# Optimization experiments

Hardware: AMD Instinct MI355X
Metric: run time of the kernel (lower is better)

The kernel has to match this reference:

```python
import jax, jax.numpy as jnp
import numpy as np
from jax import lax

EMBED = 200
HID = 300
NCLASS = 2
B = 64
S = 255          # complete binary tree: 2**8 - 1 nodes
DEPTH = 8        # levels 0..7, root at node 0
VOCAB = 32000


def make_tree():
    parent = np.zeros(S, np.int32)
    parent[0] = S  # sentinel: root has no parent (dropped via dummy segment)
    for i in range(1, S):
        parent[i] = (i - 1) // 2
    depth = np.floor(np.log2(np.arange(S) + 1)).astype(np.int32)
    return jnp.asarray(parent), jnp.asarray(depth)


def setup_inputs() -> dict:
    key = jax.random.key(0)
    ks = jax.random.split(key, 8)
    parent, depth = make_tree()
    return {
        "x": jax.random.randint(ks[0], (S, B), 0, VOCAB, dtype=jnp.int32),
        "parent": parent,
        "depth": depth,
        "embed": jax.random.normal(ks[1], (VOCAB, EMBED), jnp.float32) * 0.1,
        "W_iou": jax.random.normal(ks[2], (EMBED, 3 * HID), jnp.float32) * 0.05,
        "U_iou": jax.random.normal(ks[3], (HID, 3 * HID), jnp.float32) * 0.05,
        "b_iou": jnp.zeros((3 * HID,), jnp.float32),
        "W_f": jax.random.normal(ks[4], (EMBED, HID), jnp.float32) * 0.05,
        "U_f": jax.random.normal(ks[5], (HID, HID), jnp.float32) * 0.05,
        "b_f": jnp.zeros((HID,), jnp.float32),
        "W_out": jax.random.normal(ks[6], (HID, NCLASS), jnp.float32) * 0.05,
        "b_out": jnp.zeros((NCLASS,), jnp.float32),
    }


def reference(x, parent, depth, embed, W_iou, U_iou, b_iou, W_f, U_f, b_f, W_out, b_out):
    # x: [S, B] token ids (seq-major, as in the torch model)
    emb = embed[x]                              # [S, B, E]
    wx_iou = emb @ W_iou + b_iou                # [S, B, 3H] input contributions
    wx_f = emb @ W_f + b_f                      # [S, B, H]
    seg = jnp.minimum(parent, S)                # root -> dummy segment S
    pidx = jnp.clip(parent, 0, S - 1)           # safe gather index for parent's x-part

    H0 = jnp.zeros((S, B, HID), emb.dtype)
    C0 = jnp.zeros((S, B, HID), emb.dtype)

    def level_step(carry, d):
        H, C = carry
        child = (depth == d + 1)[:, None, None].astype(H.dtype)   # nodes feeding level d
        # child-sum of hidden states into parents
        h_sum = jax.ops.segment_sum(H * child, seg, num_segments=S + 1)[:S]  # [S,B,H]
        # per-child forget gate: sigma(W_f x_parent + U_f h_child + b_f)
        f = jax.nn.sigmoid(wx_f[pidx] + H @ U_f)                  # [S,B,H]
        fc = jax.ops.segment_sum(f * C * child, seg, num_segments=S + 1)[:S]
        iou = wx_iou + h_sum @ U_iou                              # [S,B,3H]
        i_g, o_g, u_g = jnp.split(iou, 3, axis=-1)
        i_g = jax.nn.sigmoid(i_g)
        o_g = jax.nn.sigmoid(o_g)
        u_g = jnp.tanh(u_g)
        c_new = i_g * u_g + fc
        h_new = o_g * jnp.tanh(c_new)
        node = (depth == d)[:, None, None]
        H = jnp.where(node, h_new, H)
        C = jnp.where(node, c_new, C)
        return (H, C), None

    levels = jnp.arange(DEPTH - 1, -1, -1)      # process deepest level first
    (H, C), _ = lax.scan(level_step, (H0, C0), levels)

    tree_hidden = H[0]                          # [B, H] root hidden state
    logits = tree_hidden @ W_out + b_out        # Linear(hidden_dim, n_class)
    return jax.nn.log_softmax(logits, axis=-1)  # [B, 2]
```

## Files before the change

### kernel.cpp

```cpp
#include <hip/hip_runtime.h>
#include <hip/hip_bf16.h>
#include <math.h>

#define NS 255
#define NB 64
#define NE 200
#define NH 300
#define TS 2048


typedef __attribute__((ext_vector_type(8))) short short8;
typedef __attribute__((ext_vector_type(4))) float f32x4;

__device__ __forceinline__ float sigmoidf_(float x) { return 1.0f / (1.0f + __expf(-x)); }
__device__ __forceinline__ unsigned short f2bf(float v) {
    union { __hip_bfloat16 b; unsigned short u; } cv; cv.b = __float2bfloat16(v); return cv.u;
}
__device__ __forceinline__ float bf2f(unsigned short u) {
    union { unsigned short u; __hip_bfloat16 b; } cv; cv.u = u; return __bfloat162float(cv.b);
}
__device__ __forceinline__ int swz(int row, int kk) {
    int g = (kk >> 3) ^ ((row >> 1) & 3);
    return ((row << 2) + g) * 8 + (kk & 7);
}

__global__ __launch_bounds__(256) void prep_kernel(
    const float* __restrict__ U_iou, const float* __restrict__ U_f,
    const float* __restrict__ W_iou, const float* __restrict__ W_f,
    const float* __restrict__ embed, const int* __restrict__ x,
    unsigned short* __restrict__ BW, unsigned short* __restrict__ AembT)
{
    const int nBW = 4 * 5 * 17 * TS;
    const int nAe = NS * 7 * TS;
    int total = nBW + nAe;
    int stride = gridDim.x * blockDim.x;
    for (int i = blockIdx.x * blockDim.x + threadIdx.x; i < total; i += stride) {
        if (i < nBW) {
            int e = i & (TS - 1), tile = i >> 11;
            int c = tile % 17, t2 = tile / 17;
            int s = t2 % 5, g = t2 / 5;
            int row = e >> 5, pos = (e >> 3) & 3;
            int kk = ((pos ^ ((row >> 1) & 3)) << 3) + (e & 7);
            int j = s * 64 + row;
            float v = 0.f;
            if (c < 7) {
                int k = c * 32 + kk;
                if (j < NH && k < NE) v = (g < 3) ? W_iou[k * 900 + g * NH + j] : W_f[k * NH + j];
            } else {
                int k = (c - 7) * 32 + kk;
                if (j < NH && k < NH) v = (g < 3) ? U_iou[k * 900 + g * NH + j] : U_f[k * NH + j];
            }
            BW[i] = f2bf(v);
        } else {
            int i2 = i - nBW;
            int e = i2 & (TS - 1), tile = i2 >> 11;
            int c = tile % 7, node = tile / 7;
            int row = e >> 5, pos = (e >> 3) & 3;
            int kk = ((pos ^ ((row >> 1) & 3)) << 3) + (e & 7);
            int k = c * 32 + kk;
            float v = 0.f;
            if (k < NE) v = embed[(size_t)x[node * NB + row] * NE + k];
            AembT[i2] = f2bf(v);
        }
    }
}

template<int NCH>
__device__ __forceinline__ void gemm_h(f32x4 acc[4][2],
    const unsigned short* __restrict__ A, const unsigned short* __restrict__ B,
    int offA, int offB)
{
#pragma unroll
    for (int c = 0; c < NCH; ++c) {
        const unsigned short* At = A + c * TS + offA;
        const unsigned short* Bt = B + c * TS + offB;
        short8 a0 = *(const short8*)(At);
        short8 a1 = *(const short8*)(At + 512);
#pragma unroll
        for (int t = 0; t < 4; ++t) {
            short8 b = *(const short8*)(Bt + t * 512);
            acc[t][0] = __builtin_amdgcn_mfma_f32_16x16x32_bf16(a0, b, acc[t][0], 0, 0, 0);
            acc[t][1] = __builtin_amdgcn_mfma_f32_16x16x32_bf16(a1, b, acc[t][1], 0, 0, 0);
        }
    }
}

__global__ __launch_bounds__(320) void level_kernel(
    const unsigned short* __restrict__ AembT, const unsigned short* __restrict__ BW,
    const float* __restrict__ b_iou, const float* __restrict__ b_f,
    unsigned short* __restrict__ HbfT, float* __restrict__ C,
    int base, int m, int sh)
{
    int bid = blockIdx.x;
    int p, s, half;
    if (m > 0) {
        int xcd = bid & 7, idx = bid >> 3;
        int o = idx % m, rest = idx / m;
        p = base + xcd * m + o;
        s = rest % 5; half = rest / 5;
    } else {
        int xcd = bid & 7;
        if (xcd & ((1 << sh) - 1)) return;
        p = base + (xcd >> sh);
        int idx = bid >> 3;
        s = idx % 5; half = idx / 5;
    }
    int tid = threadIdx.x;
    int w = tid >> 6, lane = tid & 63, ln = lane & 15, quad = lane >> 4;
    int l = 2 * p + 1, r = 2 * p + 2;
    int bsel = (w < 4) ? w : 3;
    int g = (quad ^ ((ln >> 1) & 3)) * 8;
    int offA = (half * 32 + ln) * 32 + g;
    int offB = ln * 32 + g;

    const unsigned short* Bsrc = BW + (size_t)(bsel * 5 + s) * 17 * TS;
    const unsigned short* Ae = AembT + (size_t)p * 7 * TS;
    const unsigned short* Hl = HbfT + (size_t)l * 10 * TS;
    const unsigned short* Hr = HbfT + (size_t)r * 10 * TS;

    f32x4 acc[4][2];
#pragma unroll
    for (int t = 0; t < 4; ++t)
#pragma unroll
        for (int q = 0; q < 2; ++q) acc[t][q] = (f32x4){0.f, 0.f, 0.f, 0.f};

    if (w < 3) {
        gemm_h<7>(acc, Ae, Bsrc, offA, offB);
        gemm_h<10>(acc, Hl, Bsrc + 7 * TS, offA, offB);
        gemm_h<10>(acc, Hr, Bsrc + 7 * TS, offA, offB);
    } else {
        gemm_h<7>(acc, Ae, Bsrc, offA, offB);
        gemm_h<10>(acc, (w == 3) ? Hl : Hr, Bsrc + 7 * TS, offA, offB);
    }

    __shared__ float tile[5][32][17];
    for (int t = 0; t < 4; ++t) {
        __syncthreads();
#pragma unroll
        for (int ms = 0; ms < 2; ++ms)
#pragma unroll
            for (int rr = 0; rr < 4; ++rr)
                tile[w][ms * 16 + quad * 4 + rr][ln] = acc[t][ms][rr];
        __syncthreads();
        for (int idx = tid; idx < 512; idx += 320) {
            int mm = idx >> 4, n = idx & 15;
            int gm = half * 32 + mm;
            int jj = s * 64 + t * 16 + n;
            bool ok = jj < NH;
            float pi = tile[0][mm][n] + (ok ? b_iou[jj] : 0.f);
            float po = tile[1][mm][n] + (ok ? b_iou[NH + jj] : 0.f);
            float pu = tile[2][mm][n] + (ok ? b_iou[2 * NH + jj] : 0.f);
            float bj = ok ? b_f[jj] : 0.f;
            float fl = sigmoidf_(tile[3][mm][n] + bj);
            float fr = sigmoidf_(tile[4][mm][n] + bj);
            float cl = ok ? C[((size_t)l * NB + gm) * NH + jj] : 0.f;
            float cr = ok ? C[((size_t)r * NB + gm) * NH + jj] : 0.f;
            float cc = sigmoidf_(pi) * tanhf(pu) + fl * cl + fr * cr;
            float hh = sigmoidf_(po) * tanhf(cc);
            if (ok) C[((size_t)p * NB + gm) * NH + jj] = cc;
            HbfT[((size_t)p * 10 + (jj >> 5)) * TS + swz(gm, jj & 31)]
                = ok ? f2bf(hh) : (unsigned short)0;
        }
    }
}

__global__ __launch_bounds__(192) void leaf_kernel(
    const unsigned short* __restrict__ AembT, const unsigned short* __restrict__ BW,
    const float* __restrict__ b_iou,
    unsigned short* __restrict__ HbfT, float* __restrict__ C, int m)
{
    int bid = blockIdx.x;
    int xcd = bid & 7, idx = bid >> 3;
    int o = idx % m, rest = idx / m;
    int p = 127 + xcd * m + o;
    int s = rest % 5, half = rest / 5;
    int tid = threadIdx.x;
    int w = tid >> 6, lane = tid & 63, ln = lane & 15, quad = lane >> 4;
    int g = (quad ^ ((ln >> 1) & 3)) * 8;
    int offA = (half * 32 + ln) * 32 + g;
    int offB = ln * 32 + g;

    const unsigned short* Bsrc = BW + (size_t)(w * 5 + s) * 17 * TS;
    const unsigned short* Ae = AembT + (size_t)p * 7 * TS;

    f32x4 acc[4][2];
#pragma unroll
    for (int t = 0; t < 4; ++t)
#pragma unroll
        for (int q = 0; q < 2; ++q) acc[t][q] = (f32x4){0.f, 0.f, 0.f, 0.f};

    gemm_h<7>(acc, Ae, Bsrc, offA, offB);

    __shared__ float tile[3][32][17];
    for (int t = 0; t < 4; ++t) {
        __syncthreads();
#pragma unroll
        for (int ms = 0; ms < 2; ++ms)
#pragma unroll
            for (int rr = 0; rr < 4; ++rr)
                tile[w][ms * 16 + quad * 4 + rr][ln] = acc[t][ms][rr];
        __syncthreads();
        for (int idx2 = tid; idx2 < 512; idx2 += 192) {
            int mm = idx2 >> 4, n = idx2 & 15;
            int gm = half * 32 + mm;
            int jj = s * 64 + t * 16 + n;
            bool ok = jj < NH;
            float pi = tile[0][mm][n] + (ok ? b_iou[jj] : 0.f);
            float po = tile[1][mm][n] + (ok ? b_iou[NH + jj] : 0.f);
            float pu = tile[2][mm][n] + (ok ? b_iou[2 * NH + jj] : 0.f);
            float cc = sigmoidf_(pi) * tanhf(pu);
            float hh = sigmoidf_(po) * tanhf(cc);
            if (ok) C[((size_t)p * NB + gm) * NH + jj] = cc;
            HbfT[((size_t)p * 10 + (jj >> 5)) * TS + swz(gm, jj & 31)]
                = ok ? f2bf(hh) : (unsigned short)0;
        }
    }
}

__global__ __launch_bounds__(64) void out_kernel(
    const unsigned short* __restrict__ HbfT,
    const float* __restrict__ W_out, const float* __restrict__ b_out,
    float* __restrict__ out)
{
    int b = threadIdx.x;
    float l0 = 0.f, l1 = 0.f;
#pragma unroll 4
    for (int k = 0; k < NH; ++k) {
        float hk = bf2f(HbfT[(size_t)(k >> 5) * TS + swz(b, k & 31)]);
        l0 += hk * W_out[k * 2];
        l1 += hk * W_out[k * 2 + 1];
    }
    l0 += b_out[0];
    l1 += b_out[1];
    float m = fmaxf(l0, l1);
    float lse = m + logf(__expf(l0 - m) + __expf(l1 - m));
    out[b * 2 + 0] = l0 - lse;
    out[b * 2 + 1] = l1 - lse;
}

extern "C" void kernel_launch(void* const* d_in, const int* in_sizes, int n_in,
                              void* d_out, int out_size, void* d_ws, size_t ws_size,
                              hipStream_t stream)
{
    const int*   x     = (const int*)d_in[0];
    const float* embed = (const float*)d_in[3];
    const float* W_iou = (const float*)d_in[4];
    const float* U_iou = (const float*)d_in[5];
    const float* b_iou = (const float*)d_in[6];
    const float* W_f   = (const float*)d_in[7];
    const float* U_f   = (const float*)d_in[8];
    const float* b_f   = (const float*)d_in[9];
    const float* W_out = (const float*)d_in[10];
    const float* b_out = (const float*)d_in[11];

    char* ws = (char*)d_ws;
    unsigned short* HbfT  = (unsigned short*)(ws + 0);
    float*          C     = (float*)(ws + 10444800);
    unsigned short* AembT = (unsigned short*)(ws + 30028800);
    unsigned short* BW    = (unsigned short*)(ws + 37340160);

    prep_kernel<<<4096, 256, 0, stream>>>(U_iou, U_f, W_iou, W_f, embed, x, BW, AembT);

    leaf_kernel<<<1280, 192, 0, stream>>>(AembT, BW, b_iou, HbfT, C, 16);
    for (int d = 6; d >= 3; --d) {
        int base = (1 << d) - 1;
        int m = 1 << (d - 3);
        level_kernel<<<80 * m, 320, 0, stream>>>(AembT, BW, b_iou, b_f, HbfT, C,
                                                 base, m, 0);
    }
    for (int d = 2; d >= 0; --d) {
        level_kernel<<<80, 320, 0, stream>>>(AembT, BW, b_iou, b_f, HbfT, C,
                                             (1 << d) - 1, 0, 3 - d);
    }
    out_kernel<<<1, 64, 0, stream>>>(HbfT, W_out, b_out, (float*)d_out);
}
```

Before: 289.2 us.

## Store cell state in fp16 tiles, stage children via LDS, vectorize prep, widen leaf tiles

```diff
diff --git a/kernel.cpp b/kernel.cpp
--- a/kernel.cpp
+++ b/kernel.cpp
@@ -7,6 +7,7 @@
 #define NE 200
 #define NH 300
 #define TS 2048
+#define HTS 1024
 
 
 typedef __attribute__((ext_vector_type(8))) short short8;
@@ -18,6 +19,12 @@
 }
 __device__ __forceinline__ float bf2f(unsigned short u) {
     union { unsigned short u; __hip_bfloat16 b; } cv; cv.u = u; return __bfloat162float(cv.b);
+}
+__device__ __forceinline__ unsigned short f2h(float v) {
+    union { _Float16 h; unsigned short u; } cv; cv.h = (_Float16)v; return cv.u;
+}
+__device__ __forceinline__ float h2f(unsigned short u) {
+    union { unsigned short u; _Float16 h; } cv; cv.u = u; return (float)cv.h;
 }
 __device__ __forceinline__ int swz(int row, int kk) {
     int g = (kk >> 3) ^ ((row >> 1) & 3);
@@ -30,50 +37,58 @@
     const float* __restrict__ embed, const int* __restrict__ x,
     unsigned short* __restrict__ BW, unsigned short* __restrict__ AembT)
 {
-    const int nBW = 4 * 5 * 17 * TS;
-    const int nAe = NS * 7 * TS;
-    int total = nBW + nAe;
+    const int gBW = 4 * 5 * 17 * 256;
+    const int gAe = NS * 7 * 256;
+    int total = gBW + gAe;
     int stride = gridDim.x * blockDim.x;
-    for (int i = blockIdx.x * blockDim.x + threadIdx.x; i < total; i += stride) {
-        if (i < nBW) {
-            int e = i & (TS - 1), tile = i >> 11;
+    for (int gi = blockIdx.x * blockDim.x + threadIdx.x; gi < total; gi += stride) {
+        unsigned short st[8];
+        if (gi < gBW) {
+            int gg = gi & 255, tile = gi >> 8;
+            int row = gg >> 2, pos = gg & 3;
+            int kk0 = (pos ^ ((row >> 1) & 3)) << 3;
             int c = tile % 17, t2 = tile / 17;
-            int s = t2 % 5, g = t2 / 5;
-            int row = e >> 5, pos = (e >> 3) & 3;
-            int kk = ((pos ^ ((row >> 1) & 3)) << 3) + (e & 7);
+            int s = t2 % 5, g4 = t2 / 5;
             int j = s * 64 + row;
-            float v = 0.f;
-            if (c < 7) {
-                int k = c * 32 + kk;
-                if (j < NH && k < NE) v = (g < 3) ? W_iou[k * 900 + g * NH + j] : W_f[k * NH + j];
-            } else {
-                int k = (c - 7) * 32 + kk;
-                if (j < NH && k < NH) v = (g < 3) ? U_iou[k * 900 + g * NH + j] : U_f[k * NH + j];
+#pragma unroll
+            for (int u = 0; u < 8; ++u) {
+                int kk = kk0 + u; float v = 0.f;
+                if (c < 7) {
+                    int k = c * 32 + kk;
+                    if (j < NH && k < NE)
+                        v = (g4 < 3) ? W_iou[k * 900 + g4 * NH + j] : W_f[k * NH + j];
+                } else {
+                    int k = (c - 7) * 32 + kk;
+                    if (j < NH && k < NH)
+                        v = (g4 < 3) ? U_iou[k * 900 + g4 * NH + j] : U_f[k * NH + j];
+                }
+                st[u] = f2bf(v);
             }
-            BW[i] = f2bf(v);
+            *(short8*)(BW + (size_t)tile * TS + (row * 4 + pos) * 8) = *(short8*)st;
         } else {
-            int i2 = i - nBW;
-            int e = i2 & (TS - 1), tile = i2 >> 11;
+            int gi2 = gi - gBW;
+            int gg = gi2 & 255, tile = gi2 >> 8;
+            int row = gg >> 2, pos = gg & 3;
+            int kk0 = (pos ^ ((row >> 1) & 3)) << 3;
             int c = tile % 7, node = tile / 7;
-            int row = e >> 5, pos = (e >> 3) & 3;
-            int kk = ((pos ^ ((row >> 1) & 3)) << 3) + (e & 7);
-            int k = c * 32 + kk;
-            float v = 0.f;
-            if (k < NE) v = embed[(size_t)x[node * NB + row] * NE + k];
-            AembT[i2] = f2bf(v);
-        }
-    }
-}
-
-template<int NCH>
-__device__ __forceinline__ void gemm_h(f32x4 acc[4][2],
-    const unsigned short* __restrict__ A, const unsigned short* __restrict__ B,
-    int offA, int offB)
+            int k0 = c * 32 + kk0;
+            const float* er = embed + (size_t)x[node * NB + row] * NE;
+#pragma unroll
+            for (int u = 0; u < 8; ++u)
+                st[u] = (k0 + u < NE) ? f2bf(er[k0 + u]) : (unsigned short)0;
+            *(short8*)(AembT + (size_t)tile * TS + (row * 4 + pos) * 8) = *(short8*)st;
+        }
+    }
+}
+
+template<int NCH, int SA>
+__device__ __forceinline__ void gemm2(f32x4 acc[4][2],
+    const unsigned short* __restrict__ A, const unsigned short* __restrict__ B)
 {
 #pragma unroll
     for (int c = 0; c < NCH; ++c) {
-        const unsigned short* At = A + c * TS + offA;
-        const unsigned short* Bt = B + c * TS + offB;
+        const unsigned short* At = A + c * SA;
+        const unsigned short* Bt = B + c * TS;
         short8 a0 = *(const short8*)(At);
         short8 a1 = *(const short8*)(At + 512);
 #pragma unroll
@@ -84,13 +99,36 @@
         }
     }
 }
+template<int NCH>
+__device__ __forceinline__ void gemm_f(f32x4 acc[4][4],
+    const unsigned short* __restrict__ A, const unsigned short* __restrict__ B)
+{
+#pragma unroll
+    for (int c = 0; c < NCH; ++c) {
+        const unsigned short* At = A + c * TS;
+        const unsigned short* Bt = B + c * TS;
+        short8 a0 = *(const short8*)(At);
+        short8 a1 = *(const short8*)(At + 512);
+        short8 a2 = *(const short8*)(At + 1024);
+        short8 a3 = *(const short8*)(At + 1536);
+#pragma unroll
+        for (int t = 0; t < 4; ++t) {
+            short8 b = *(const short8*)(Bt + t * 512);
+            acc[t][0] = __builtin_amdgcn_mfma_f32_16x16x32_bf16(a0, b, acc[t][0], 0, 0, 0);
+            acc[t][1] = __builtin_amdgcn_mfma_f32_16x16x32_bf16(a1, b, acc[t][1], 0, 0, 0);
+            acc[t][2] = __builtin_amdgcn_mfma_f32_16x16x32_bf16(a2, b, acc[t][2], 0, 0, 0);
+            acc[t][3] = __builtin_amdgcn_mfma_f32_16x16x32_bf16(a3, b, acc[t][3], 0, 0, 0);
+        }
+    }
+}
 
 __global__ __launch_bounds__(320) void level_kernel(
     const unsigned short* __restrict__ AembT, const unsigned short* __restrict__ BW,
     const float* __restrict__ b_iou, const float* __restrict__ b_f,
-    unsigned short* __restrict__ HbfT, float* __restrict__ C,
+    unsigned short* __restrict__ HbfT, unsigned short* __restrict__ Cg,
     int base, int m, int sh)
 {
+    __shared__ unsigned short sm[24 * HTS];
     int bid = blockIdx.x;
     int p, s, half;
     if (m > 0) {
@@ -109,57 +147,83 @@
     int w = tid >> 6, lane = tid & 63, ln = lane & 15, quad = lane >> 4;
     int l = 2 * p + 1, r = 2 * p + 2;
     int bsel = (w < 4) ? w : 3;
-    int g = (quad ^ ((ln >> 1) & 3)) * 8;
-    int offA = (half * 32 + ln) * 32 + g;
-    int offB = ln * 32 + g;
+    int gq = (quad ^ ((ln >> 1) & 3)) * 8;
+    int offA = (half * 32 + ln) * 32 + gq;
+    int offL = ln * 32 + gq;
+    int offB = ln * 32 + gq;
+
+    for (int idx = w; idx < 24; idx += 5) {
+        const unsigned short* gsrc;
+        if (idx < 20) {
+            int node = (idx < 10) ? l : r;
+            int tt = (idx < 10) ? idx : idx - 10;
+            gsrc = HbfT + ((size_t)node * 10 + tt) * TS + half * HTS;
+        } else {
+            int ii = idx - 20;
+            int node = (ii < 2) ? l : r;
+            gsrc = Cg + ((size_t)node * 10 + 2 * s + (ii & 1)) * TS + half * HTS;
+        }
+        unsigned short* ldst = sm + idx * HTS;
+#pragma unroll
+        for (int u = 0; u < 2; ++u)
+            __builtin_amdgcn_global_load_lds(
+                (const __attribute__((address_space(1))) unsigned short*)(gsrc + u * 512 + lane * 8),
+                (__attribute__((address_space(3))) unsigned short*)(ldst + u * 512 + lane * 8),
+                16, 0, 0);
+    }
+
+    f32x4 acc[4][2];
+#pragma unroll
+    for (int t = 0; t < 4; ++t)
+#pragma unroll
+        for (int q = 0; q < 2; ++q) acc[t][q] = (f32x4){0.f, 0.f, 0.f, 0.f};
 
     const unsigned short* Bsrc = BW + (size_t)(bsel * 5 + s) * 17 * TS;
     const unsigned short* Ae = AembT + (size_t)p * 7 * TS;
-    const unsigned short* Hl = HbfT + (size_t)l * 10 * TS;
-    const unsigned short* Hr = HbfT + (size_t)r * 10 * TS;
-
-    f32x4 acc[4][2];
-#pragma unroll
-    for (int t = 0; t < 4; ++t)
-#pragma unroll
-        for (int q = 0; q < 2; ++q) acc[t][q] = (f32x4){0.f, 0.f, 0.f, 0.f};
-
+    gemm2<7, TS>(acc, Ae + offA, Bsrc + offB);
+
+    __syncthreads();
+
+    const unsigned short* BH = Bsrc + 7 * TS + offB;
     if (w < 3) {
-        gemm_h<7>(acc, Ae, Bsrc, offA, offB);
-        gemm_h<10>(acc, Hl, Bsrc + 7 * TS, offA, offB);
-        gemm_h<10>(acc, Hr, Bsrc + 7 * TS, offA, offB);
+        gemm2<10, HTS>(acc, sm + offL, BH);
+        gemm2<10, HTS>(acc, sm + 10 * HTS + offL, BH);
+    } else if (w == 3) {
+        gemm2<10, HTS>(acc, sm + offL, BH);
     } else {
-        gemm_h<7>(acc, Ae, Bsrc, offA, offB);
-        gemm_h<10>(acc, (w == 3) ? Hl : Hr, Bsrc + 7 * TS, offA, offB);
-    }
-
-    __shared__ float tile[5][32][17];
+        gemm2<10, HTS>(acc, sm + 10 * HTS + offL, BH);
+    }
+
+    float* smf = (float*)sm;
     for (int t = 0; t < 4; ++t) {
         __syncthreads();
 #pragma unroll
         for (int ms = 0; ms < 2; ++ms)
 #pragma unroll
             for (int rr = 0; rr < 4; ++rr)
-                tile[w][ms * 16 + quad * 4 + rr][ln] = acc[t][ms][rr];
+                smf[w * 544 + (ms * 16 + quad * 4 + rr) * 17 + ln] = acc[t][ms][rr];
         __syncthreads();
-        for (int idx = tid; idx < 512; idx += 320) {
-            int mm = idx >> 4, n = idx & 15;
+        for (int idx2 = tid; idx2 < 512; idx2 += 320) {
+            int mm = idx2 >> 4, n = idx2 & 15;
             int gm = half * 32 + mm;
             int jj = s * 64 + t * 16 + n;
             bool ok = jj < NH;
-            float pi = tile[0][mm][n] + (ok ? b_iou[jj] : 0.f);
-            float po = tile[1][mm][n] + (ok ? b_iou[NH + jj] : 0.f);
-            float pu = tile[2][mm][n] + (ok ? b_iou[2 * NH + jj] : 0.f);
+            float pi = smf[0 * 544 + mm * 17 + n] + (ok ? b_iou[jj] : 0.f);
+            float po = smf[1 * 544 + mm * 17 + n] + (ok ? b_iou[NH + jj] : 0.f);
+            float pu = smf[2 * 544 + mm * 17 + n] + (ok ? b_iou[2 * NH + jj] : 0.f);
             float bj = ok ? b_f[jj] : 0.f;
-            float fl = sigmoidf_(tile[3][mm][n] + bj);
-            float fr = sigmoidf_(tile[4][mm][n] + bj);
-            float cl = ok ? C[((size_t)l * NB + gm) * NH + jj] : 0.f;
-            float cr = ok ? C[((size_t)r * NB + gm) * NH + jj] : 0.f;
+            float fl = sigmoidf_(smf[3 * 544 + mm * 17 + n] + bj);
+            float fr = sigmoidf_(smf[4 * 544 + mm * 17 + n] + bj);
+            int xr = (mm >> 1) & 3;
+            int cel = (mm * 4 + ((((t & 1) * 2) + (n >> 3)) ^ xr)) * 8 + (n & 7);
+            int ts2 = t >> 1;
+            float cl = h2f(sm[(20 + ts2) * HTS + cel]);
+            float cr = h2f(sm[(22 + ts2) * HTS + cel]);
             float cc = sigmoidf_(pi) * tanhf(pu) + fl * cl + fr * cr;
             float hh = sigmoidf_(po) * tanhf(cc);
-            if (ok) C[((size_t)p * NB + gm) * NH + jj] = cc;
-            HbfT[((size_t)p * 10 + (jj >> 5)) * TS + swz(gm, jj & 31)]
-                = ok ? f2bf(hh) : (unsigned short)0;
+            size_t tbase = ((size_t)p * 10 + (jj >> 5)) * TS + swz(gm, jj & 31);
+            if (ok) Cg[tbase] = f2h(cc);
+            HbfT[tbase] = ok ? f2bf(hh) : (unsigned short)0;
         }
     }
 }
@@ -167,42 +231,39 @@
 __global__ __launch_bounds__(192) void leaf_kernel(
     const unsigned short* __restrict__ AembT, const unsigned short* __restrict__ BW,
     const float* __restrict__ b_iou,
-    unsigned short* __restrict__ HbfT, float* __restrict__ C, int m)
+    unsigned short* __restrict__ HbfT, unsigned short* __restrict__ Cg, int m)
 {
     int bid = blockIdx.x;
     int xcd = bid & 7, idx = bid >> 3;
     int o = idx % m, rest = idx / m;
     int p = 127 + xcd * m + o;
-    int s = rest % 5, half = rest / 5;
+    int s = rest % 5;
     int tid = threadIdx.x;
     int w = tid >> 6, lane = tid & 63, ln = lane & 15, quad = lane >> 4;
-    int g = (quad ^ ((ln >> 1) & 3)) * 8;
-    int offA = (half * 32 + ln) * 32 + g;
-    int offB = ln * 32 + g;
+    int off = ln * 32 + (quad ^ ((ln >> 1) & 3)) * 8;
 
     const unsigned short* Bsrc = BW + (size_t)(w * 5 + s) * 17 * TS;
     const unsigned short* Ae = AembT + (size_t)p * 7 * TS;
 
-    f32x4 acc[4][2];
+    f32x4 acc[4][4];
 #pragma unroll
     for (int t = 0; t < 4; ++t)
 #pragma unroll
-        for (int q = 0; q < 2; ++q) acc[t][q] = (f32x4){0.f, 0.f, 0.f, 0.f};
-
-    gemm_h<7>(acc, Ae, Bsrc, offA, offB);
-
-    __shared__ float tile[3][32][17];
+        for (int q = 0; q < 4; ++q) acc[t][q] = (f32x4){0.f, 0.f, 0.f, 0.f};
+
+    gemm_f<7>(acc, Ae + off, Bsrc + off);
+
+    __shared__ float tile[3][64][16];
     for (int t = 0; t < 4; ++t) {
         __syncthreads();
 #pragma unroll
-        for (int ms = 0; ms < 2; ++ms)
+        for (int ms = 0; ms < 4; ++ms)
 #pragma unroll
             for (int rr = 0; rr < 4; ++rr)
                 tile[w][ms * 16 + quad * 4 + rr][ln] = acc[t][ms][rr];
         __syncthreads();
-        for (int idx2 = tid; idx2 < 512; idx2 += 192) {
+        for (int idx2 = tid; idx2 < 1024; idx2 += 192) {
             int mm = idx2 >> 4, n = idx2 & 15;
-            int gm = half * 32 + mm;
             int jj = s * 64 + t * 16 + n;
             bool ok = jj < NH;
             float pi = tile[0][mm][n] + (ok ? b_iou[jj] : 0.f);
@@ -210,9 +271,9 @@
             float pu = tile[2][mm][n] + (ok ? b_iou[2 * NH + jj] : 0.f);
             float cc = sigmoidf_(pi) * tanhf(pu);
             float hh = sigmoidf_(po) * tanhf(cc);
-            if (ok) C[((size_t)p * NB + gm) * NH + jj] = cc;
-            HbfT[((size_t)p * 10 + (jj >> 5)) * TS + swz(gm, jj & 31)]
-                = ok ? f2bf(hh) : (unsigned short)0;
+            size_t tbase = ((size_t)p * 10 + (jj >> 5)) * TS + swz(mm, jj & 31);
+            if (ok) Cg[tbase] = f2h(cc);
+            HbfT[tbase] = ok ? f2bf(hh) : (unsigned short)0;
         }
     }
 }
@@ -255,21 +316,21 @@
 
     char* ws = (char*)d_ws;
     unsigned short* HbfT  = (unsigned short*)(ws + 0);
-    float*          C     = (float*)(ws + 10444800);
-    unsigned short* AembT = (unsigned short*)(ws + 30028800);
-    unsigned short* BW    = (unsigned short*)(ws + 37340160);
+    unsigned short* Cg    = (unsigned short*)(ws + 10444800);
+    unsigned short* AembT = (unsigned short*)(ws + 20889600);
+    unsigned short* BW    = (unsigned short*)(ws + 28200960);
 
     prep_kernel<<<4096, 256, 0, stream>>>(U_iou, U_f, W_iou, W_f, embed, x, BW, AembT);
 
-    leaf_kernel<<<1280, 192, 0, stream>>>(AembT, BW, b_iou, HbfT, C, 16);
+    leaf_kernel<<<640, 192, 0, stream>>>(AembT, BW, b_iou, HbfT, Cg, 16);
     for (int d = 6; d >= 3; --d) {
         int base = (1 << d) - 1;
         int m = 1 << (d - 3);
-        level_kernel<<<80 * m, 320, 0, stream>>>(AembT, BW, b_iou, b_f, HbfT, C,
+        level_kernel<<<80 * m, 320, 0, stream>>>(AembT, BW, b_iou, b_f, HbfT, Cg,
                                                  base, m, 0);
     }
     for (int d = 2; d >= 0; --d) {
-        level_kernel<<<80, 320, 0, stream>>>(AembT, BW, b_iou, b_f, HbfT, C,
+        level_kernel<<<80, 320, 0, stream>>>(AembT, BW, b_iou, b_f, HbfT, Cg,
                                              (1 << d) - 1, 0, 3 - d);
     }
     out_kernel<<<1, 64, 0, stream>>>(HbfT, W_out, b_out, (float*)d_out);
```

New measurement: 274.9 us. 4.9% less time.
